# Kernel tuning notes

Measured on AMD Instinct MI355X. Metric: run time of the kernel, lower is better.

Reference implementation:

```python
import jax, jax.numpy as jnp
import numpy as np

S, B, H, N = 512, 32, 512, 131072  # seq_len, batch, hidden_dim, num candidate spans
MAX_STEP = 20  # max_length


def setup_inputs() -> dict:
    key = jax.random.key(0)
    ks = jax.random.split(key, 8)
    hidden = jax.random.normal(ks[0], (S, B, 2 * H), dtype=jnp.float32)
    span_bids = jax.random.randint(ks[1], (N,), 0, B, dtype=jnp.int32)
    # begin in [1, S-1-MAX_STEP-1] so that begin-1>=0 and end=begin+step <= S-1
    span_begins = jax.random.randint(ks[2], (N,), 1, S - MAX_STEP - 2, dtype=jnp.int32)
    steps = jax.random.randint(ks[3], (N,), 2, MAX_STEP + 1, dtype=jnp.int32)
    span_ends = span_begins + steps
    span_flags = jax.random.randint(ks[4], (N,), 0, 2, dtype=jnp.int32)
    span_weights = jax.random.uniform(ks[5], (N,), dtype=jnp.float32)
    W1 = jax.random.normal(ks[6], (2 * H, H), dtype=jnp.float32) / np.sqrt(2.0 * H)
    b1 = jnp.zeros((H,), dtype=jnp.float32)
    W2 = jax.random.normal(ks[7], (H, 1), dtype=jnp.float32) / np.sqrt(float(H))
    b2 = jnp.zeros((1,), dtype=jnp.float32)
    return {"hidden": hidden, "span_bids": span_bids, "span_begins": span_begins,
            "span_ends": span_ends, "span_flags": span_flags, "span_weights": span_weights,
            "W1": W1, "b1": b1, "W2": W2, "b2": b2}


def reference(hidden, span_bids, span_begins, span_ends, span_flags, span_weights, W1, b1, W2, b2):
    h = W2.shape[0]  # hidden_dim
    # vectorized _span_embed: fwd diff on first half, bwd diff on second half
    fwd = hidden[span_ends - 1, span_bids, :h] - hidden[span_begins - 1, span_bids, :h]
    bwd = hidden[span_begins, span_bids, h:] - hidden[span_ends, span_bids, h:]
    feats = jnp.concatenate([fwd, bwd], axis=-1)  # [N, 2H]
    z = jnp.maximum(feats @ W1 + b1, 0.0)
    p = jax.nn.sigmoid(z @ W2 + b2)[:, 0]  # [N]
    targets = (span_flags == 1).astype(p.dtype)
    n_pos = jnp.sum(targets)
    n_tot = jnp.asarray(targets.shape[0], p.dtype)
    scale = 2.0 * n_pos / n_tot  # negative weights scaled by 2*P/(P+N)
    w_eff = jnp.where(span_flags == 1, span_weights, span_weights * scale)
    pc = jnp.clip(p, 1e-7, 1.0 - 1e-7)
    bce = -(targets * jnp.log(pc) + (1.0 - targets) * jnp.log(1.0 - pc))
    loss = jnp.mean(w_eff * bce)
    return loss
```

## Files before the change

### kernel.cpp

```cpp
#include <hip/hip_runtime.h>
#include <hip/hip_bf16.h>


typedef float f32x4 __attribute__((ext_vector_type(4)));
typedef float f32x2 __attribute__((ext_vector_type(2)));
typedef __bf16 bf16x8 __attribute__((ext_vector_type(8)));

__device__ __forceinline__ unsigned short f2bf(float f) {
  unsigned int u = __float_as_uint(f);
  u += 0x7fffu + ((u >> 16) & 1u);
  return (unsigned short)(u >> 16);
}
__device__ __forceinline__ float bf2f(unsigned int lo16) {
  return __uint_as_float(lo16 << 16);
}

__global__ void w1_blocked(const float* __restrict__ W1,
                           unsigned short* __restrict__ W1b) {
  int idx = blockIdx.x * 256 + threadIdx.x;
  int kc = idx & 3;
  int n  = (idx >> 2) & 511;
  int c  = idx >> 11;
  int k0 = c * 32 + kc * 8;
  unsigned short tmp[8];
#pragma unroll
  for (int j = 0; j < 8; ++j)
    tmp[j] = f2bf(W1[(k0 + j) * 512 + n]);
  *(uint4*)(W1b + c * 16384 + n * 32 + kc * 8) = *(uint4*)tmp;
}

#define APITCH 520
__global__ __launch_bounds__(256, 2) void proj_gemm(
    const float* __restrict__ hidden,
    const unsigned short* __restrict__ w1b,
    unsigned char* __restrict__ Wq) {
  __shared__ __align__(16) unsigned short AH[64 * APITCH];
  unsigned short* Eb = AH;

  const int t = threadIdx.x;
  const int lane = t & 63;
  const int w = t >> 6;
  const int r0 = blockIdx.x << 6;
  const int hk = blockIdx.y << 9;
  const int q = lane >> 4;
  const int m = lane & 15;

  {
    const int col = (t & 31) << 4;
    const int rsub = t >> 5;
#pragma unroll
    for (int p = 0; p < 8; ++p) {
      int row = (p << 3) + rsub;
      const float4* gp = (const float4*)(hidden + ((r0 + row) << 10) + hk + col);
      float4 f0 = gp[0], f1 = gp[1], f2 = gp[2], f3 = gp[3];
      uint4 a, b;
      a.x = (unsigned)f2bf(f0.x) | ((unsigned)f2bf(f0.y) << 16);
      a.y = (unsigned)f2bf(f0.z) | ((unsigned)f2bf(f0.w) << 16);
      a.z = (unsigned)f2bf(f1.x) | ((unsigned)f2bf(f1.y) << 16);
      a.w = (unsigned)f2bf(f1.z) | ((unsigned)f2bf(f1.w) << 16);
      b.x = (unsigned)f2bf(f2.x) | ((unsigned)f2bf(f2.y) << 16);
      b.y = (unsigned)f2bf(f2.z) | ((unsigned)f2bf(f2.w) << 16);
      b.z = (unsigned)f2bf(f3.x) | ((unsigned)f2bf(f3.y) << 16);
      b.w = (unsigned)f2bf(f3.z) | ((unsigned)f2bf(f3.w) << 16);
      unsigned short* dst = AH + row * APITCH + col;
      *(uint4*)dst = a;
      *(uint4*)(dst + 8) = b;
    }
  }
  __syncthreads();

  int boffn[8];
#pragma unroll
  for (int nt = 0; nt < 8; ++nt)
    boffn[nt] = (((w << 7) + (nt << 4) + m) << 5) + (q << 3);
  const unsigned short* w1base = w1b + (blockIdx.y << 18);

  f32x4 acc[4][8];
#pragma unroll
  for (int i = 0; i < 4; ++i)
#pragma unroll
    for (int j = 0; j < 8; ++j) acc[i][j] = (f32x4){0.f, 0.f, 0.f, 0.f};

#pragma unroll
  for (int it = 0; it < 16; ++it) {
    const unsigned short* bt = w1base + (it << 14);
    bf16x8 bfr[8];
#pragma unroll
    for (int nt = 0; nt < 8; ++nt)
      bfr[nt] = *(const bf16x8*)(bt + boffn[nt]);
    bf16x8 af[4];
#pragma unroll
    for (int mt = 0; mt < 4; ++mt)
      af[mt] = *(const bf16x8*)(AH + ((mt << 4) + m) * APITCH + (it << 5) + (q << 3));
#pragma unroll
    for (int mt = 0; mt < 4; ++mt)
#pragma unroll
      for (int nt = 0; nt < 8; ++nt)
        acc[mt][nt] = __builtin_amdgcn_mfma_f32_16x16x32_bf16(af[mt], bfr[nt],
                                                              acc[mt][nt], 0, 0, 0);
  }
  __syncthreads();

#pragma unroll
  for (int pass = 0; pass < 2; ++pass) {
#pragma unroll
    for (int mh = 0; mh < 2; ++mh) {
      int mt = (pass << 1) + mh;
#pragma unroll
      for (int r = 0; r < 4; ++r) {
        int rr = (mh << 4) + ((lane >> 4) << 2) + r;
#pragma unroll
        for (int nt = 0; nt < 8; ++nt)
          Eb[((w << 5) + rr) * 136 + (nt << 4) + (lane & 15)] = f2bf(acc[mt][nt][r]);
      }
    }
#pragma unroll
    for (int i = 0; i < 8; ++i) {
      int task = (i << 6) + lane;
      int rr = task >> 4;
      int ck = task & 15;
      uint4 v = *(const uint4*)&Eb[((w << 5) + rr) * 136 + (ck << 3)];
      float f0 = bf2f(v.x & 0xffff), f1 = bf2f(v.x >> 16);
      float f2 = bf2f(v.y & 0xffff), f3 = bf2f(v.y >> 16);
      float f4 = bf2f(v.z & 0xffff), f5 = bf2f(v.z >> 16);
      float f6 = bf2f(v.w & 0xffff), f7 = bf2f(v.w >> 16);
      uint2 o;
      o.x = __builtin_amdgcn_cvt_pk_fp8_f32(f0, f1, 0, false);
      o.x = __builtin_amdgcn_cvt_pk_fp8_f32(f2, f3, o.x, true);
      o.y = __builtin_amdgcn_cvt_pk_fp8_f32(f4, f5, 0, false);
      o.y = __builtin_amdgcn_cvt_pk_fp8_f32(f6, f7, o.y, true);
      int grow = r0 + (pass << 5) + rr;
      int col = (w << 7) + (ck << 3);
      if (hk == 0) {
        *(uint2*)(Wq + (grow << 10) + col) = o;
      } else if (grow >= 32) {
        *(uint2*)(Wq + ((grow - 32) << 10) + 512 + col) = o;
      }
    }
  }
}

#define SPB 64
__global__ __launch_bounds__(256) void span_eval(
    const unsigned char* __restrict__ Wq,
    const int* __restrict__ bids, const int* __restrict__ begins,
    const int* __restrict__ ends, const int* __restrict__ flags,
    const float* __restrict__ weights,
    const float* __restrict__ b1, const float* __restrict__ w2,
    const float* __restrict__ b2, float* __restrict__ partials) {
  __shared__ int oB[SPB], oE[SPB], sfl[SPB];
  __shared__ float swt[SPB];
  __shared__ float red[4][3];
  const int t = threadIdx.x;
  const int lane = t & 63;
  const int w = t >> 6;
  const int h = lane >> 5;
  const int hl = lane & 31;
  const int sbase = blockIdx.x * SPB;

  if (t < SPB) {
    int s = sbase + t;
    int b = bids[s], bg = begins[s], en = ends[s];
    oB[t] = (((bg - 1) << 5) + b) << 10;
    oE[t] = (((en - 1) << 5) + b) << 10;
    sfl[t] = flags[s];
    swt[t] = weights[s];
  }
  __syncthreads();

  const int sp0 = ((w << 1) + h) << 3;
  const int c0 = hl << 4;
  float b1v[16], w2v[16];
#pragma unroll
  for (int q = 0; q < 4; ++q) {
    float4 bv = *(const float4*)(b1 + c0 + (q << 2));
    float4 wv = *(const float4*)(w2 + c0 + (q << 2));
    b1v[(q << 2) + 0] = bv.x; b1v[(q << 2) + 1] = bv.y;
    b1v[(q << 2) + 2] = bv.z; b1v[(q << 2) + 3] = bv.w;
    w2v[(q << 2) + 0] = wv.x; w2v[(q << 2) + 1] = wv.y;
    w2v[(q << 2) + 2] = wv.z; w2v[(q << 2) + 3] = wv.w;
  }

  auto dec = [](unsigned int v, float* f) {
    f32x2 a = __builtin_amdgcn_cvt_pk_f32_fp8(v, false);
    f32x2 b = __builtin_amdgcn_cvt_pk_f32_fp8(v, true);
    f[0] = a[0]; f[1] = a[1]; f[2] = b[0]; f[3] = b[1];
  };

  uint4 BU[3], BV[3], EU[3], EV[3];
  auto ld = [&](int slot, int j) {
    int ob = oB[sp0 + j], oe = oE[sp0 + j];
    BU[slot] = *(const uint4*)(Wq + ob + c0);
    BV[slot] = *(const uint4*)(Wq + ob + 512 + c0);
    EU[slot] = *(const uint4*)(Wq + oe + c0);
    EV[slot] = *(const uint4*)(Wq + oe + 512 + c0);
  };
  ld(0, 0); ld(1, 1); ld(2, 2);

  float mylogit = 0.f;
#pragma unroll
  for (int j = 0; j < 8; ++j) {
    const int slot = j % 3;
    float buf[16], bvf[16], euf[16], evf[16];
    dec(BU[slot].x, buf); dec(BU[slot].y, buf + 4);
    dec(BU[slot].z, buf + 8); dec(BU[slot].w, buf + 12);
    dec(BV[slot].x, bvf); dec(BV[slot].y, bvf + 4);
    dec(BV[slot].z, bvf + 8); dec(BV[slot].w, bvf + 12);
    dec(EU[slot].x, euf); dec(EU[slot].y, euf + 4);
    dec(EU[slot].z, euf + 8); dec(EU[slot].w, euf + 12);
    dec(EV[slot].x, evf); dec(EV[slot].y, evf + 4);
    dec(EV[slot].z, evf + 8); dec(EV[slot].w, evf + 12);
    if (j + 3 < 8) ld(slot, j + 3);
    float sv = 0.f;
#pragma unroll
    for (int k = 0; k < 16; ++k) {
      float zp = euf[k] - buf[k] + bvf[k] - evf[k] + b1v[k];
      sv += fmaxf(zp, 0.f) * w2v[k];
    }
    sv += __shfl_xor(sv, 1);
    sv += __shfl_xor(sv, 2);
    sv += __shfl_xor(sv, 4);
    sv += __shfl_xor(sv, 8);
    sv += __shfl_xor(sv, 16);
    if (hl == j) mylogit = sv;
  }

  mylogit = __shfl(mylogit, ((lane & 8) << 2) + (lane & 7));

  float pos_t = 0.f, neg_t = 0.f, cnt_t = 0.f;
  if (lane < 16) {
    int sl = (w << 4) + lane;
    float logit = mylogit + b2[0];
    float p = 1.f / (1.f + expf(-logit));
    p = fminf(fmaxf(p, 1e-7f), 1.f - 1e-7f);
    int fl = sfl[sl];
    float bce = (fl == 1) ? -logf(p) : -logf(1.f - p);
    float term = swt[sl] * bce;
    pos_t = (fl == 1) ? term : 0.f;
    neg_t = (fl == 1) ? 0.f : term;
    cnt_t = (fl == 1) ? 1.f : 0.f;
  }
#pragma unroll
  for (int off = 1; off < 64; off <<= 1) {
    pos_t += __shfl_xor(pos_t, off);
    neg_t += __shfl_xor(neg_t, off);
    cnt_t += __shfl_xor(cnt_t, off);
  }
  if (lane == 0) { red[w][0] = pos_t; red[w][1] = neg_t; red[w][2] = cnt_t; }
  __syncthreads();
  if (t == 0) {
    partials[(blockIdx.x << 2) + 0] = red[0][0] + red[1][0] + red[2][0] + red[3][0];
    partials[(blockIdx.x << 2) + 1] = red[0][1] + red[1][1] + red[2][1] + red[3][1];
    partials[(blockIdx.x << 2) + 2] = red[0][2] + red[1][2] + red[2][2] + red[3][2];
  }
}

__global__ void finalize(const float* __restrict__ parts, int nblk,
                         float* __restrict__ out, int nspans) {
  __shared__ float sp[4], sn[4], sc[4];
  float P = 0.f, Ng = 0.f, C = 0.f;
  for (int i = threadIdx.x; i < nblk; i += 256) {
    P += parts[(i << 2) + 0];
    Ng += parts[(i << 2) + 1];
    C += parts[(i << 2) + 2];
  }
#pragma unroll
  for (int off = 1; off < 64; off <<= 1) {
    P += __shfl_xor(P, off);
    Ng += __shfl_xor(Ng, off);
    C += __shfl_xor(C, off);
  }
  int w = threadIdx.x >> 6;
  if ((threadIdx.x & 63) == 0) { sp[w] = P; sn[w] = Ng; sc[w] = C; }
  __syncthreads();
  if (threadIdx.x == 0) {
    P = sp[0] + sp[1] + sp[2] + sp[3];
    Ng = sn[0] + sn[1] + sn[2] + sn[3];
    C = sc[0] + sc[1] + sc[2] + sc[3];
    float scale = 2.f * C / (float)nspans;
    out[0] = (P + scale * Ng) / (float)nspans;
  }
}

extern "C" void kernel_launch(void* const* d_in, const int* in_sizes, int n_in,
                              void* d_out, int out_size, void* d_ws, size_t ws_size,
                              hipStream_t stream) {
  const float* hidden = (const float*)d_in[0];
  const int* bids     = (const int*)d_in[1];
  const int* begins   = (const int*)d_in[2];
  const int* ends     = (const int*)d_in[3];
  const int* flags    = (const int*)d_in[4];
  const float* weights = (const float*)d_in[5];
  const float* W1 = (const float*)d_in[6];
  const float* b1 = (const float*)d_in[7];
  const float* W2 = (const float*)d_in[8];
  const float* b2 = (const float*)d_in[9];
  float* out = (float*)d_out;
  const int nspans = in_sizes[1];
  const int nblk = nspans / SPB;

  float* partials = (float*)d_ws;
  unsigned short* W1b = (unsigned short*)((char*)d_ws + (1 << 18));
  unsigned char* Wq = (unsigned char*)((char*)d_ws + (2 << 20));

  w1_blocked<<<256, 256, 0, stream>>>(W1, W1b);
  proj_gemm<<<dim3(256, 2), 256, 0, stream>>>(hidden, W1b, Wq);
  span_eval<<<nblk, 256, 0, stream>>>(Wq, bids, begins, ends, flags, weights,
                                      b1, W2, b2, partials);
  finalize<<<1, 256, 0, stream>>>(partials, nblk, out, nspans);
}
```

Measured before the change: 175.3 us.

## Bucket spans by batch and begin position; halve proj_gemm row tile

Adds a three-kernel counting sort (histogram, scan, scatter) that groups spans by batch id and coarse begin position. It writes packed offset, flag and weight metadata so span_eval blocks gather from nearby rows of the projected matrix, which should improve cache locality. Separately, proj_gemm now uses 32-row tiles with half the accumulators, twice as many blocks and a higher occupancy target. The cost is three extra launches and a pass over the span arrays, plus a smaller GEMM tile with less reuse of W1.

```diff
diff --git a/kernel.cpp b/kernel.cpp
--- a/kernel.cpp
+++ b/kernel.cpp
@@ -29,18 +29,88 @@
   *(uint4*)(W1b + c * 16384 + n * 32 + kc * 8) = *(uint4*)tmp;
 }
 
+__global__ __launch_bounds__(256) void sort_hist(
+    const int* __restrict__ bids, const int* __restrict__ begins,
+    int* __restrict__ g) {
+  __shared__ int h[1024];
+  const int t = threadIdx.x;
+  for (int j = t; j < 1024; j += 256) h[j] = 0;
+  __syncthreads();
+  int base = blockIdx.x * 4096;
+#pragma unroll 4
+  for (int k = 0; k < 16; ++k) {
+    int s = base + (k << 8) + t;
+    int bin = (bids[s] << 5) | (begins[s] >> 4);
+    atomicAdd(&h[bin], 1);
+  }
+  __syncthreads();
+  for (int j = t; j < 1024; j += 256) g[blockIdx.x * 1024 + j] = h[j];
+}
+
+__global__ __launch_bounds__(256) void sort_scan(int* __restrict__ g) {
+  __shared__ int wt[4];
+  const int t = threadIdx.x, lane = t & 63, w = t >> 6;
+  const int b0 = t << 2;
+  int tot0 = 0, tot1 = 0, tot2 = 0, tot3 = 0;
+  for (int i = 0; i < 32; ++i) {
+    int4 v = *(const int4*)(g + i * 1024 + b0);
+    tot0 += v.x; tot1 += v.y; tot2 += v.z; tot3 += v.w;
+  }
+  int lsum = tot0 + tot1 + tot2 + tot3;
+  int ts = lsum;
+#pragma unroll
+  for (int off = 1; off < 64; off <<= 1) {
+    int n = __shfl_up(ts, off);
+    if (lane >= off) ts += n;
+  }
+  if (lane == 63) wt[w] = ts;
+  __syncthreads();
+  int wbase = 0;
+  for (int i = 0; i < w; ++i) wbase += wt[i];
+  int r0 = wbase + ts - lsum;
+  int r1 = r0 + tot0, r2 = r1 + tot1, r3 = r2 + tot2;
+  for (int i = 0; i < 32; ++i) {
+    int4 v = *(const int4*)(g + i * 1024 + b0);
+    *(int4*)(g + i * 1024 + b0) = make_int4(r0, r1, r2, r3);
+    r0 += v.x; r1 += v.y; r2 += v.z; r3 += v.w;
+  }
+}
+
+__global__ __launch_bounds__(256) void sort_scatter(
+    const int* __restrict__ bids, const int* __restrict__ begins,
+    const int* __restrict__ ends, const int* __restrict__ flags,
+    const float* __restrict__ weights, const int* __restrict__ g,
+    int4* __restrict__ smeta) {
+  __shared__ int cur[1024];
+  const int t = threadIdx.x;
+  for (int j = t; j < 1024; j += 256) cur[j] = g[blockIdx.x * 1024 + j];
+  __syncthreads();
+  int base = blockIdx.x * 4096;
+#pragma unroll 4
+  for (int k = 0; k < 16; ++k) {
+    int s = base + (k << 8) + t;
+    int b = bids[s], bg = begins[s], en = ends[s];
+    int bin = (b << 5) | (bg >> 4);
+    int slot = atomicAdd(&cur[bin], 1);
+    smeta[slot] = make_int4((((bg - 1) << 5) + b) << 10,
+                            (((en - 1) << 5) + b) << 10,
+                            flags[s], __float_as_int(weights[s]));
+  }
+}
+
 #define APITCH 520
-__global__ __launch_bounds__(256, 2) void proj_gemm(
+__global__ __launch_bounds__(256, 4) void proj_gemm(
     const float* __restrict__ hidden,
     const unsigned short* __restrict__ w1b,
     unsigned char* __restrict__ Wq) {
-  __shared__ __align__(16) unsigned short AH[64 * APITCH];
-  unsigned short* Eb = AH;
+  __shared__ __align__(16) char smem[34816];
+  unsigned short* AH = (unsigned short*)smem;
+  unsigned short* Eb = (unsigned short*)smem;
 
   const int t = threadIdx.x;
   const int lane = t & 63;
   const int w = t >> 6;
-  const int r0 = blockIdx.x << 6;
+  const int r0 = blockIdx.x << 5;
   const int hk = blockIdx.y << 9;
   const int q = lane >> 4;
   const int m = lane & 15;
@@ -49,7 +119,7 @@
     const int col = (t & 31) << 4;
     const int rsub = t >> 5;
 #pragma unroll
-    for (int p = 0; p < 8; ++p) {
+    for (int p = 0; p < 4; ++p) {
       int row = (p << 3) + rsub;
       const float4* gp = (const float4*)(hidden + ((r0 + row) << 10) + hk + col);
       float4 f0 = gp[0], f1 = gp[1], f2 = gp[2], f3 = gp[3];
@@ -75,9 +145,9 @@
     boffn[nt] = (((w << 7) + (nt << 4) + m) << 5) + (q << 3);
   const unsigned short* w1base = w1b + (blockIdx.y << 18);
 
-  f32x4 acc[4][8];
-#pragma unroll
-  for (int i = 0; i < 4; ++i)
+  f32x4 acc[2][8];
+#pragma unroll
+  for (int i = 0; i < 2; ++i)
 #pragma unroll
     for (int j = 0; j < 8; ++j) acc[i][j] = (f32x4){0.f, 0.f, 0.f, 0.f};
 
@@ -88,64 +158,53 @@
 #pragma unroll
     for (int nt = 0; nt < 8; ++nt)
       bfr[nt] = *(const bf16x8*)(bt + boffn[nt]);
-    bf16x8 af[4];
-#pragma unroll
-    for (int mt = 0; mt < 4; ++mt)
-      af[mt] = *(const bf16x8*)(AH + ((mt << 4) + m) * APITCH + (it << 5) + (q << 3));
-#pragma unroll
-    for (int mt = 0; mt < 4; ++mt)
+    bf16x8 af0 = *(const bf16x8*)(AH + m * APITCH + (it << 5) + (q << 3));
+    bf16x8 af1 = *(const bf16x8*)(AH + (16 + m) * APITCH + (it << 5) + (q << 3));
+#pragma unroll
+    for (int nt = 0; nt < 8; ++nt) {
+      acc[0][nt] = __builtin_amdgcn_mfma_f32_16x16x32_bf16(af0, bfr[nt], acc[0][nt], 0, 0, 0);
+      acc[1][nt] = __builtin_amdgcn_mfma_f32_16x16x32_bf16(af1, bfr[nt], acc[1][nt], 0, 0, 0);
+    }
+  }
+  __syncthreads();
+
+#pragma unroll
+  for (int mt = 0; mt < 2; ++mt)
+#pragma unroll
+    for (int r = 0; r < 4; ++r) {
+      int rr = (mt << 4) + ((lane >> 4) << 2) + r;
 #pragma unroll
       for (int nt = 0; nt < 8; ++nt)
-        acc[mt][nt] = __builtin_amdgcn_mfma_f32_16x16x32_bf16(af[mt], bfr[nt],
-                                                              acc[mt][nt], 0, 0, 0);
-  }
-  __syncthreads();
-
-#pragma unroll
-  for (int pass = 0; pass < 2; ++pass) {
-#pragma unroll
-    for (int mh = 0; mh < 2; ++mh) {
-      int mt = (pass << 1) + mh;
-#pragma unroll
-      for (int r = 0; r < 4; ++r) {
-        int rr = (mh << 4) + ((lane >> 4) << 2) + r;
-#pragma unroll
-        for (int nt = 0; nt < 8; ++nt)
-          Eb[((w << 5) + rr) * 136 + (nt << 4) + (lane & 15)] = f2bf(acc[mt][nt][r]);
-      }
-    }
-#pragma unroll
-    for (int i = 0; i < 8; ++i) {
-      int task = (i << 6) + lane;
-      int rr = task >> 4;
-      int ck = task & 15;
-      uint4 v = *(const uint4*)&Eb[((w << 5) + rr) * 136 + (ck << 3)];
-      float f0 = bf2f(v.x & 0xffff), f1 = bf2f(v.x >> 16);
-      float f2 = bf2f(v.y & 0xffff), f3 = bf2f(v.y >> 16);
-      float f4 = bf2f(v.z & 0xffff), f5 = bf2f(v.z >> 16);
-      float f6 = bf2f(v.w & 0xffff), f7 = bf2f(v.w >> 16);
-      uint2 o;
-      o.x = __builtin_amdgcn_cvt_pk_fp8_f32(f0, f1, 0, false);
-      o.x = __builtin_amdgcn_cvt_pk_fp8_f32(f2, f3, o.x, true);
-      o.y = __builtin_amdgcn_cvt_pk_fp8_f32(f4, f5, 0, false);
-      o.y = __builtin_amdgcn_cvt_pk_fp8_f32(f6, f7, o.y, true);
-      int grow = r0 + (pass << 5) + rr;
-      int col = (w << 7) + (ck << 3);
-      if (hk == 0) {
-        *(uint2*)(Wq + (grow << 10) + col) = o;
-      } else if (grow >= 32) {
-        *(uint2*)(Wq + ((grow - 32) << 10) + 512 + col) = o;
-      }
+        Eb[((w << 5) + rr) * 136 + (nt << 4) + (lane & 15)] = f2bf(acc[mt][nt][r]);
+    }
+#pragma unroll
+  for (int i = 0; i < 8; ++i) {
+    int task = (i << 6) + lane;
+    int rr = task >> 4;
+    int ck = task & 15;
+    uint4 v = *(const uint4*)&Eb[((w << 5) + rr) * 136 + (ck << 3)];
+    float f0 = bf2f(v.x & 0xffff), f1 = bf2f(v.x >> 16);
+    float f2 = bf2f(v.y & 0xffff), f3 = bf2f(v.y >> 16);
+    float f4 = bf2f(v.z & 0xffff), f5 = bf2f(v.z >> 16);
+    float f6 = bf2f(v.w & 0xffff), f7 = bf2f(v.w >> 16);
+    uint2 o;
+    o.x = __builtin_amdgcn_cvt_pk_fp8_f32(f0, f1, 0, false);
+    o.x = __builtin_amdgcn_cvt_pk_fp8_f32(f2, f3, o.x, true);
+    o.y = __builtin_amdgcn_cvt_pk_fp8_f32(f4, f5, 0, false);
+    o.y = __builtin_amdgcn_cvt_pk_fp8_f32(f6, f7, o.y, true);
+    int grow = r0 + rr;
+    int col = (w << 7) + (ck << 3);
+    if (hk == 0) {
+      *(uint2*)(Wq + (grow << 10) + col) = o;
+    } else if (grow >= 32) {
+      *(uint2*)(Wq + ((grow - 32) << 10) + 512 + col) = o;
     }
   }
 }
 
 #define SPB 64
 __global__ __launch_bounds__(256) void span_eval(
-    const unsigned char* __restrict__ Wq,
-    const int* __restrict__ bids, const int* __restrict__ begins,
-    const int* __restrict__ ends, const int* __restrict__ flags,
-    const float* __restrict__ weights,
+    const unsigned char* __restrict__ Wq, const int4* __restrict__ smeta,
     const float* __restrict__ b1, const float* __restrict__ w2,
     const float* __restrict__ b2, float* __restrict__ partials) {
   __shared__ int oB[SPB], oE[SPB], sfl[SPB];
@@ -159,12 +218,11 @@
   const int sbase = blockIdx.x * SPB;
 
   if (t < SPB) {
-    int s = sbase + t;
-    int b = bids[s], bg = begins[s], en = ends[s];
-    oB[t] = (((bg - 1) << 5) + b) << 10;
-    oE[t] = (((en - 1) << 5) + b) << 10;
-    sfl[t] = flags[s];
-    swt[t] = weights[s];
+    int4 mt = smeta[sbase + t];
+    oB[t] = mt.x;
+    oE[t] = mt.y;
+    sfl[t] = mt.z;
+    swt[t] = __int_as_float(mt.w);
   }
   __syncthreads();
 
@@ -172,13 +230,13 @@
   const int c0 = hl << 4;
   float b1v[16], w2v[16];
 #pragma unroll
-  for (int q = 0; q < 4; ++q) {
-    float4 bv = *(const float4*)(b1 + c0 + (q << 2));
-    float4 wv = *(const float4*)(w2 + c0 + (q << 2));
-    b1v[(q << 2) + 0] = bv.x; b1v[(q << 2) + 1] = bv.y;
-    b1v[(q << 2) + 2] = bv.z; b1v[(q << 2) + 3] = bv.w;
-    w2v[(q << 2) + 0] = wv.x; w2v[(q << 2) + 1] = wv.y;
-    w2v[(q << 2) + 2] = wv.z; w2v[(q << 2) + 3] = wv.w;
+  for (int qq = 0; qq < 4; ++qq) {
+    float4 bv = *(const float4*)(b1 + c0 + (qq << 2));
+    float4 wv = *(const float4*)(w2 + c0 + (qq << 2));
+    b1v[(qq << 2) + 0] = bv.x; b1v[(qq << 2) + 1] = bv.y;
+    b1v[(qq << 2) + 2] = bv.z; b1v[(qq << 2) + 3] = bv.w;
+    w2v[(qq << 2) + 0] = wv.x; w2v[(qq << 2) + 1] = wv.y;
+    w2v[(qq << 2) + 2] = wv.z; w2v[(qq << 2) + 3] = wv.w;
   }
 
   auto dec = [](unsigned int v, float* f) {
@@ -301,11 +359,16 @@
 
   float* partials = (float*)d_ws;
   unsigned short* W1b = (unsigned short*)((char*)d_ws + (1 << 18));
+  int* ghist = (int*)((char*)d_ws + (3 << 19));
   unsigned char* Wq = (unsigned char*)((char*)d_ws + (2 << 20));
+  int4* smeta = (int4*)((char*)d_ws + (20 << 20));
 
   w1_blocked<<<256, 256, 0, stream>>>(W1, W1b);
-  proj_gemm<<<dim3(256, 2), 256, 0, stream>>>(hidden, W1b, Wq);
-  span_eval<<<nblk, 256, 0, stream>>>(Wq, bids, begins, ends, flags, weights,
-                                      b1, W2, b2, partials);
+  sort_hist<<<32, 256, 0, stream>>>(bids, begins, ghist);
+  sort_scan<<<1, 256, 0, stream>>>(ghist);
+  sort_scatter<<<32, 256, 0, stream>>>(bids, begins, ends, flags, weights,
+                                       ghist, smeta);
+  proj_gemm<<<dim3(512, 2), 256, 0, stream>>>(hidden, W1b, Wq);
+  span_eval<<<nblk, 256, 0, stream>>>(Wq, smeta, b1, W2, b2, partials);
   finalize<<<1, 256, 0, stream>>>(partials, nblk, out, nspans);
 }
```

New measurement: 196.7 us. 1.12x slower.
